# Performance work log

Measured on AMD Instinct MI355X. Metric: run time of the kernel, lower is better.

Reference implementation:

```python
import jax, jax.numpy as jnp
import numpy as np

N_NODE = 100000
HIDDEN = 128
BATCH = 4096
SESS_LEN = 50


def setup_inputs() -> dict:
    key = jax.random.key(0)
    k1, k2, k3, k4, k5 = jax.random.split(key, 5)
    return {
        "item_embedding": jax.random.normal(k1, (N_NODE, HIDDEN), dtype=jnp.float32),
        "items": jax.random.randint(k2, (BATCH, SESS_LEN), 0, N_NODE, dtype=jnp.int64),
        "A": jax.random.uniform(k3, (BATCH, BATCH), dtype=jnp.float32),
        "D": jax.random.uniform(k4, (BATCH, BATCH), dtype=jnp.float32),
        "target_embedding": jax.random.normal(k5, (BATCH, 1, 2 * HIDDEN), dtype=jnp.float32),
    }


def reference(item_embedding, items, A, D, target_embedding):
    # Gather per-session item embeddings: (batch, sess_len, hidden)
    seq_h = item_embedding[items]
    # Sum over session positions -> (batch, hidden)
    relation_emb = jnp.sum(seq_h, axis=1)
    # DA = D @ A, then propagate: (batch, batch) @ (batch, hidden)
    DA = jnp.matmul(D, A)
    relation_emb = jnp.matmul(DA, relation_emb)
    # Row-wise L2 normalization (torch.norm(dim=-1))
    norm = jnp.linalg.norm(relation_emb, axis=-1, keepdims=True)
    return relation_emb / norm
```

## Files before the change

kernel.cpp:

```cpp
#include <hip/hip_runtime.h>
#include <hip/hip_bf16.h>

#define BATCH   4096
#define HIDDEN  128
#define SESS    50
#define KTOT    4096
#define NB      ((size_t)BATCH * HIDDEN)

typedef __bf16 bf16x8 __attribute__((ext_vector_type(8)));
typedef float  f32x4  __attribute__((ext_vector_type(4)));
typedef unsigned char uchar;

__device__ __forceinline__ f32x4 mfma_bf16(bf16x8 a, bf16x8 b, f32x4 c) {
    return __builtin_amdgcn_mfma_f32_16x16x32_bf16(a, b, c, 0, 0, 0);
}

__device__ __forceinline__ long packBH(int k, int h) {
    return ((long)(k >> 3) << 10) + ((h >> 4) << 7) + ((h & 15) << 3) + (k & 7);
}

__global__ __launch_bounds__(64)
void probe_kernel(int* __restrict__ flag, uchar* __restrict__ rtab,
                  uchar* __restrict__ ctab) {
    __shared__ float As[16][32];
    __shared__ float Bs[32][16];
    __shared__ int cnt[256];
    const int lane = threadIdx.x;
    for (int idx = lane; idx < 512; idx += 64) {
        const int m = idx >> 5, k = idx & 31;
        As[m][k] = (float)(((m * 5 + k * 3) % 17) - 8);
        const int kb = idx >> 4, n = idx & 15;
        Bs[kb][n] = (float)(((kb * 7 + n * 11) % 17) - 8);
    }
    for (int i = lane; i < 256; i += 64) cnt[i] = 0;
    __syncthreads();

    const int lo = lane & 15, quad = lane >> 4;
    bf16x8 a, b, a1, b1, a2, b2;
#pragma unroll
    for (int j = 0; j < 8; ++j) {
        a[j]  = (__bf16)As[lo][quad * 8 + j];
        b[j]  = (__bf16)Bs[quad * 8 + j][lo];
        a1[j] = (__bf16)0.f; b1[j] = (__bf16)0.f;
        a2[j] = (__bf16)0.f; b2[j] = (__bf16)0.f;
    }
    if (quad == 0) {
        a1[0] = (__bf16)(float)lo;  b1[0] = (__bf16)1.f;
        a2[0] = (__bf16)1.f;        b2[0] = (__bf16)(float)lo;
    }
    const f32x4 z = {0.f, 0.f, 0.f, 0.f};
    f32x4 d  = mfma_bf16(a,  b,  z);
    f32x4 d1 = mfma_bf16(a1, b1, z);
    f32x4 d2 = mfma_bf16(a2, b2, z);

    bool ok = true;
    int ms[4], ns[4];
#pragma unroll
    for (int r = 0; r < 4; ++r) {
        const int m = (int)d1[r], n = (int)d2[r];
        ok = ok && ((float)m == d1[r]) && ((float)n == d2[r]) &&
             (m >= 0) && (m < 16) && (n >= 0) && (n < 16);
        ms[r] = m & 15; ns[r] = n & 15;
        float ref = 0.f;
        for (int k = 0; k < 32; ++k) ref += As[ms[r]][k] * Bs[k][ns[r]];
        ok = ok && (d[r] == ref);
        atomicAdd(&cnt[ms[r] * 16 + ns[r]], 1);
    }
    __syncthreads();
    bool comp = true;
    for (int i = lane; i < 256; i += 64) comp = comp && (cnt[i] == 1);

    const unsigned long long b_ok   = __ballot(ok);
    const unsigned long long b_comp = __ballot(comp);
#pragma unroll
    for (int r = 0; r < 4; ++r) {
        rtab[lane * 4 + r] = (uchar)ms[r];
        ctab[lane * 4 + r] = (uchar)ns[r];
    }
    if (lane == 0)
        *flag = (b_ok == ~0ULL && b_comp == ~0ULL) ? 1 : 0;
}

__global__ __launch_bounds__(256)
void gather_sum_kernel(const float* __restrict__ emb,
                       const int* __restrict__ items32,
                       float* __restrict__ Ef,
                       __bf16* __restrict__ ETp) {
    __shared__ int sidx[2][SESS];
    __shared__ f32x4 red[2][4][32];
    const int t  = threadIdx.x;
    const int b0 = blockIdx.x * 2;
    const bool is64 = (items32[1] | items32[3] | items32[5] | items32[7] |
                       items32[9] | items32[11] | items32[13] | items32[15]) == 0;
    if (t < 2 * SESS) {
        sidx[t / SESS][t % SESS] =
            is64 ? (int)((const long long*)items32)[(long)b0 * SESS + t]
                 : items32[b0 * SESS + t];
    }
    __syncthreads();
    const int r  = t >> 7;
    const int g  = (t >> 5) & 3;
    const int c4 = (t & 31) * 4;
    f32x4 acc = {0.f, 0.f, 0.f, 0.f};
#pragma unroll
    for (int s = g; s < SESS; s += 4) {
        acc += *(const f32x4*)(emb + (long)sidx[r][s] * HIDDEN + c4);
    }
    red[r][g][t & 31] = acc;
    __syncthreads();
    if (g == 0) {
        const int b = b0 + r;
        const f32x4 v = red[r][0][t & 31] + red[r][1][t & 31] +
                        red[r][2][t & 31] + red[r][3][t & 31];
        *(f32x4*)(Ef + (long)b * HIDDEN + c4) = v;
        const long pb = ((long)(b >> 3) << 10) + (b & 7) + ((c4 >> 4) << 7);
#pragma unroll
        for (int j = 0; j < 4; ++j)
            ETp[pb + ((c4 & 15) + j) * 8] = (__bf16)v[j];
    }
}

template <int PHASE>
__global__ __launch_bounds__(256, 4)
void gemm_mfma_kernel(const float* __restrict__ X,
                      const __bf16* __restrict__ BTp,
                      const int* __restrict__ flag,
                      const uchar* __restrict__ rtab,
                      const uchar* __restrict__ ctab,
                      float* __restrict__ Tp,
                      float* __restrict__ RpX) {
    if (*flag != 1) return;
    __shared__ float red[4][16][128];

    const int tid  = threadIdx.x;
    const int wave = tid >> 6;
    const int lane = tid & 63;
    const int lo   = lane & 15;
    const int quad = lane >> 4;
    const int rowBase = blockIdx.x * 16;
    const int sy      = blockIdx.y;
    const int kBase   = sy * 1024 + wave * 256;

    const unsigned rt4 = ((const unsigned*)rtab)[lane];
    const unsigned ct4 = ((const unsigned*)ctab)[lane];

    f32x4 acc[8];
#pragma unroll
    for (int i = 0; i < 8; ++i) acc[i] = (f32x4){0.f, 0.f, 0.f, 0.f};

    const float*  ap = X + (long)(rowBase + lo) * KTOT + kBase + quad * 8;
    const __bf16* bp = BTp + (((long)(kBase >> 3) + quad) << 10) + lo * 8;

    f32x4 x0 = *(const f32x4*)(ap);
    f32x4 x1 = *(const f32x4*)(ap + 4);
    bf16x8 bb[8];
#pragma unroll
    for (int nt = 0; nt < 8; ++nt)
        bb[nt] = *(const bf16x8*)(bp + nt * 128);

#pragma unroll
    for (int it = 0; it < 7; ++it) {
        const float*  ap2 = ap + (it + 1) * 32;
        const __bf16* bp2 = bp + (long)(it + 1) * 4096;
        const f32x4 nx0 = *(const f32x4*)(ap2);
        const f32x4 nx1 = *(const f32x4*)(ap2 + 4);
        bf16x8 nb[8];
#pragma unroll
        for (int nt = 0; nt < 8; ++nt)
            nb[nt] = *(const bf16x8*)(bp2 + nt * 128);
        bf16x8 a;
        a[0] = (__bf16)x0[0]; a[1] = (__bf16)x0[1];
        a[2] = (__bf16)x0[2]; a[3] = (__bf16)x0[3];
        a[4] = (__bf16)x1[0]; a[5] = (__bf16)x1[1];
        a[6] = (__bf16)x1[2]; a[7] = (__bf16)x1[3];
#pragma unroll
        for (int nt = 0; nt < 8; ++nt)
            acc[nt] = mfma_bf16(a, bb[nt], acc[nt]);
        x0 = nx0; x1 = nx1;
#pragma unroll
        for (int nt = 0; nt < 8; ++nt) bb[nt] = nb[nt];
    }
    {
        bf16x8 a;
        a[0] = (__bf16)x0[0]; a[1] = (__bf16)x0[1];
        a[2] = (__bf16)x0[2]; a[3] = (__bf16)x0[3];
        a[4] = (__bf16)x1[0]; a[5] = (__bf16)x1[1];
        a[6] = (__bf16)x1[2]; a[7] = (__bf16)x1[3];
#pragma unroll
        for (int nt = 0; nt < 8; ++nt)
            acc[nt] = mfma_bf16(a, bb[nt], acc[nt]);
    }

#pragma unroll
    for (int r = 0; r < 4; ++r) {
        const int dr = (rt4 >> (8 * r)) & 255;
        const int dc = (ct4 >> (8 * r)) & 255;
#pragma unroll
        for (int nt = 0; nt < 8; ++nt)
            red[wave][dr][nt * 16 + dc] = acc[nt][r];
    }
    __syncthreads();

    float* outp = (PHASE == 1) ? (Tp + (size_t)sy * NB)
                               : (sy < 3 ? Tp + (size_t)(sy + 1) * NB : RpX);
    const int row = tid >> 4;
    const int cb  = (tid & 15) * 8;
    f32x4 v0, v1;
#pragma unroll
    for (int j = 0; j < 4; ++j) {
        v0[j] = red[0][row][cb + j] + red[1][row][cb + j] +
                red[2][row][cb + j] + red[3][row][cb + j];
        v1[j] = red[0][row][cb + 4 + j] + red[1][row][cb + 4 + j] +
                red[2][row][cb + 4 + j] + red[3][row][cb + 4 + j];
    }
    *(f32x4*)(outp + (long)(rowBase + row) * HIDDEN + cb)     = v0;
    *(f32x4*)(outp + (long)(rowBase + row) * HIDDEN + cb + 4) = v1;
}

template <int PHASE>
__global__ __launch_bounds__(256)
void gemm_fp32_kernel(const float* __restrict__ X,
                      const float* __restrict__ B,
                      const int* __restrict__ flag,
                      float* __restrict__ Tp,
                      float* __restrict__ RpX) {
    if (*flag == 1) return;
    const int tid = threadIdx.x;
    const int cg4 = (tid & 31) * 4;
    const int rg  = tid >> 5;
    const int r0  = blockIdx.x * 32 + rg * 4;
    const int sy  = blockIdx.y;
    const int ks  = sy * 1024;
    float* outp = (PHASE == 1) ? (Tp + (size_t)sy * NB)
                               : (sy < 3 ? Tp + (size_t)(sy + 1) * NB : RpX);

    f32x4 acc[4];
#pragma unroll
    for (int j = 0; j < 4; ++j) acc[j] = (f32x4){0.f, 0.f, 0.f, 0.f};

    const float* Bp = B + (long)ks * HIDDEN + cg4;
    const float* Xp = X + (long)r0 * KTOT + ks;

    for (int k = 0; k < 1024; k += 4) {
        const f32x4 b0 = *(const f32x4*)(Bp + (long)(k + 0) * HIDDEN);
        const f32x4 b1 = *(const f32x4*)(Bp + (long)(k + 1) * HIDDEN);
        const f32x4 b2 = *(const f32x4*)(Bp + (long)(k + 2) * HIDDEN);
        const f32x4 b3 = *(const f32x4*)(Bp + (long)(k + 3) * HIDDEN);
#pragma unroll
        for (int j = 0; j < 4; ++j) {
            const f32x4 x = *(const f32x4*)(Xp + (long)j * KTOT + k);
            acc[j] += x[0] * b0;
            acc[j] += x[1] * b1;
            acc[j] += x[2] * b2;
            acc[j] += x[3] * b3;
        }
    }
#pragma unroll
    for (int j = 0; j < 4; ++j)
        *(f32x4*)(outp + (long)(r0 + j) * HIDDEN + cg4) = acc[j];
}

__global__ __launch_bounds__(256)
void reduce4_kernel(float* __restrict__ Tp, __bf16* __restrict__ TTp) {
    const size_t i = ((size_t)blockIdx.x * 256 + threadIdx.x) * 4;
    f32x4 a = *(const f32x4*)(Tp + i);
    a += *(const f32x4*)(Tp + NB + i);
    a += *(const f32x4*)(Tp + 2 * NB + i);
    a += *(const f32x4*)(Tp + 3 * NB + i);
    *(f32x4*)(Tp + i) = a;
    const int b  = (int)(i >> 7);
    const int h0 = (int)(i & 127);
    const long pb = ((long)(b >> 3) << 10) + (b & 7) + ((h0 >> 4) << 7);
#pragma unroll
    for (int j = 0; j < 4; ++j)
        TTp[pb + ((h0 & 15) + j) * 8] = (__bf16)a[j];
}

__global__ __launch_bounds__(128)
void reduce_norm_kernel(const float* __restrict__ Tp,
                        const float* __restrict__ RpX,
                        float* __restrict__ out) {
    __shared__ float s[128];
    const int row = blockIdx.x;
    const int h   = threadIdx.x;
    const size_t i = (size_t)row * HIDDEN + h;
    const float v = Tp[NB + i] + Tp[2 * NB + i] + Tp[3 * NB + i] + RpX[i];
    s[h] = v * v;
    __syncthreads();
#pragma unroll
    for (int o = 64; o > 0; o >>= 1) {
        if (h < o) s[h] += s[h + o];
        __syncthreads();
    }
    out[i] = v * rsqrtf(s[0]);
}

extern "C" void kernel_launch(void* const* d_in, const int* in_sizes, int n_in,
                              void* d_out, int out_size, void* d_ws, size_t ws_size,
                              hipStream_t stream) {
    const float* emb   = (const float*)d_in[0];
    const int*   items = (const int*)d_in[1];
    const float* A     = (const float*)d_in[2];
    const float* D     = (const float*)d_in[3];
    float* out = (float*)d_out;

    uchar* base = (uchar*)d_ws;
    int*   flag = (int*)base;
    uchar* rtab = base + 64;
    uchar* ctab = base + 320;
    float*  Ef  = (float*)(base + 1024);
    __bf16* ETp = (__bf16*)(Ef + NB);
    __bf16* TTp = ETp + NB;
    float*  Tp  = (float*)(TTp + NB);
    float*  RpX = Tp + 4 * NB;

    probe_kernel<<<1, 64, 0, stream>>>(flag, rtab, ctab);
    gather_sum_kernel<<<BATCH / 2, 256, 0, stream>>>(emb, items, Ef, ETp);

    gemm_mfma_kernel<1><<<dim3(BATCH / 16, 4), 256, 0, stream>>>(A, ETp, flag, rtab, ctab, Tp, RpX);
    gemm_fp32_kernel<1><<<dim3(BATCH / 32, 4), 256, 0, stream>>>(A, Ef, flag, Tp, RpX);
    reduce4_kernel<<<512, 256, 0, stream>>>(Tp, TTp);

    gemm_mfma_kernel<2><<<dim3(BATCH / 16, 4), 256, 0, stream>>>(D, TTp, flag, rtab, ctab, Tp, RpX);
    gemm_fp32_kernel<2><<<dim3(BATCH / 32, 4), 256, 0, stream>>>(D, Tp, flag, Tp, RpX);
    reduce_norm_kernel<<<BATCH, 128, 0, stream>>>(Tp, RpX, out);
}
```

Baseline: 238.4 us.

## Drop MFMA probe and fp32 fallback, stage B via global_load_lds double buffering

Removes the runtime MFMA layout probe kernel and its flag-gated fp32 fallback GEMMs, hardcoding the 16x16x32 bf16 output layout. The GEMM now streams the packed bf16 B operand into LDS with async global_load_lds in a two-stage double buffer, using explicit waitcnt control to overlap loads with MFMAs. Gather-sum, reduce4 and the final norm kernel are also reworked to use wave shuffles instead of LDS reductions, and redundant fp32 outputs are no longer written. The cost is 64KB of LDS per block, with occupancy lowered to 2, and the loss of the fallback path if the assumed MFMA layout is wrong.

```diff
diff --git a/kernel.cpp b/kernel.cpp
--- a/kernel.cpp
+++ b/kernel.cpp
@@ -9,129 +9,61 @@
 
 typedef __bf16 bf16x8 __attribute__((ext_vector_type(8)));
 typedef float  f32x4  __attribute__((ext_vector_type(4)));
-typedef unsigned char uchar;
+typedef float  f32x2  __attribute__((ext_vector_type(2)));
 
 __device__ __forceinline__ f32x4 mfma_bf16(bf16x8 a, bf16x8 b, f32x4 c) {
     return __builtin_amdgcn_mfma_f32_16x16x32_bf16(a, b, c, 0, 0, 0);
 }
 
-__device__ __forceinline__ long packBH(int k, int h) {
-    return ((long)(k >> 3) << 10) + ((h >> 4) << 7) + ((h & 15) << 3) + (k & 7);
-}
-
-__global__ __launch_bounds__(64)
-void probe_kernel(int* __restrict__ flag, uchar* __restrict__ rtab,
-                  uchar* __restrict__ ctab) {
-    __shared__ float As[16][32];
-    __shared__ float Bs[32][16];
-    __shared__ int cnt[256];
-    const int lane = threadIdx.x;
-    for (int idx = lane; idx < 512; idx += 64) {
-        const int m = idx >> 5, k = idx & 31;
-        As[m][k] = (float)(((m * 5 + k * 3) % 17) - 8);
-        const int kb = idx >> 4, n = idx & 15;
-        Bs[kb][n] = (float)(((kb * 7 + n * 11) % 17) - 8);
-    }
-    for (int i = lane; i < 256; i += 64) cnt[i] = 0;
-    __syncthreads();
-
-    const int lo = lane & 15, quad = lane >> 4;
-    bf16x8 a, b, a1, b1, a2, b2;
-#pragma unroll
-    for (int j = 0; j < 8; ++j) {
-        a[j]  = (__bf16)As[lo][quad * 8 + j];
-        b[j]  = (__bf16)Bs[quad * 8 + j][lo];
-        a1[j] = (__bf16)0.f; b1[j] = (__bf16)0.f;
-        a2[j] = (__bf16)0.f; b2[j] = (__bf16)0.f;
-    }
-    if (quad == 0) {
-        a1[0] = (__bf16)(float)lo;  b1[0] = (__bf16)1.f;
-        a2[0] = (__bf16)1.f;        b2[0] = (__bf16)(float)lo;
-    }
-    const f32x4 z = {0.f, 0.f, 0.f, 0.f};
-    f32x4 d  = mfma_bf16(a,  b,  z);
-    f32x4 d1 = mfma_bf16(a1, b1, z);
-    f32x4 d2 = mfma_bf16(a2, b2, z);
-
-    bool ok = true;
-    int ms[4], ns[4];
-#pragma unroll
-    for (int r = 0; r < 4; ++r) {
-        const int m = (int)d1[r], n = (int)d2[r];
-        ok = ok && ((float)m == d1[r]) && ((float)n == d2[r]) &&
-             (m >= 0) && (m < 16) && (n >= 0) && (n < 16);
-        ms[r] = m & 15; ns[r] = n & 15;
-        float ref = 0.f;
-        for (int k = 0; k < 32; ++k) ref += As[ms[r]][k] * Bs[k][ns[r]];
-        ok = ok && (d[r] == ref);
-        atomicAdd(&cnt[ms[r] * 16 + ns[r]], 1);
-    }
-    __syncthreads();
-    bool comp = true;
-    for (int i = lane; i < 256; i += 64) comp = comp && (cnt[i] == 1);
-
-    const unsigned long long b_ok   = __ballot(ok);
-    const unsigned long long b_comp = __ballot(comp);
-#pragma unroll
-    for (int r = 0; r < 4; ++r) {
-        rtab[lane * 4 + r] = (uchar)ms[r];
-        ctab[lane * 4 + r] = (uchar)ns[r];
-    }
-    if (lane == 0)
-        *flag = (b_ok == ~0ULL && b_comp == ~0ULL) ? 1 : 0;
-}
+__device__ __forceinline__ void gload16(const void* g, void* l) {
+    __builtin_amdgcn_global_load_lds(
+        (const __attribute__((address_space(1))) void*)g,
+        (__attribute__((address_space(3))) void*)l, 16, 0, 0);
+}
+
 
 __global__ __launch_bounds__(256)
 void gather_sum_kernel(const float* __restrict__ emb,
                        const int* __restrict__ items32,
-                       float* __restrict__ Ef,
                        __bf16* __restrict__ ETp) {
-    __shared__ int sidx[2][SESS];
-    __shared__ f32x4 red[2][4][32];
+    __shared__ int sidx[4][SESS];
     const int t  = threadIdx.x;
-    const int b0 = blockIdx.x * 2;
+    const int b0 = blockIdx.x * 4;
     const bool is64 = (items32[1] | items32[3] | items32[5] | items32[7] |
                        items32[9] | items32[11] | items32[13] | items32[15]) == 0;
-    if (t < 2 * SESS) {
-        sidx[t / SESS][t % SESS] =
-            is64 ? (int)((const long long*)items32)[(long)b0 * SESS + t]
-                 : items32[b0 * SESS + t];
+    if (t < 4 * SESS) {
+        const int w_ = t / SESS, s_ = t % SESS;
+        sidx[w_][s_] = is64
+            ? (int)((const long long*)items32)[(long)(b0 + w_) * SESS + s_]
+            : items32[(b0 + w_) * SESS + s_];
     }
     __syncthreads();
-    const int r  = t >> 7;
-    const int g  = (t >> 5) & 3;
-    const int c4 = (t & 31) * 4;
+    const int w    = t >> 6;
+    const int lane = t & 63;
+    const int c    = lane & 31;
+    const int h    = lane >> 5;
     f32x4 acc = {0.f, 0.f, 0.f, 0.f};
 #pragma unroll
-    for (int s = g; s < SESS; s += 4) {
-        acc += *(const f32x4*)(emb + (long)sidx[r][s] * HIDDEN + c4);
-    }
-    red[r][g][t & 31] = acc;
-    __syncthreads();
-    if (g == 0) {
-        const int b = b0 + r;
-        const f32x4 v = red[r][0][t & 31] + red[r][1][t & 31] +
-                        red[r][2][t & 31] + red[r][3][t & 31];
-        *(f32x4*)(Ef + (long)b * HIDDEN + c4) = v;
-        const long pb = ((long)(b >> 3) << 10) + (b & 7) + ((c4 >> 4) << 7);
+    for (int i = 0; i < 25; ++i) {
+        acc += *(const f32x4*)(emb + (long)sidx[w][h + 2 * i] * HIDDEN + c * 4);
+    }
+#pragma unroll
+    for (int j = 0; j < 4; ++j) acc[j] += __shfl_xor(acc[j], 32, 64);
+    if (h == 0) {
+        const int b  = b0 + w;
+        const int h0 = c * 4;
+        const long pb = ((long)(b >> 3) << 10) + (b & 7) + ((h0 >> 4) << 7);
 #pragma unroll
         for (int j = 0; j < 4; ++j)
-            ETp[pb + ((c4 & 15) + j) * 8] = (__bf16)v[j];
-    }
-}
-
-template <int PHASE>
-__global__ __launch_bounds__(256, 4)
+            ETp[pb + ((h0 & 15) + j) * 8] = (__bf16)acc[j];
+    }
+}
+
+__global__ __launch_bounds__(256, 2)
 void gemm_mfma_kernel(const float* __restrict__ X,
-                      const __bf16* __restrict__ BTp,
-                      const int* __restrict__ flag,
-                      const uchar* __restrict__ rtab,
-                      const uchar* __restrict__ ctab,
-                      float* __restrict__ Tp,
-                      float* __restrict__ RpX) {
-    if (*flag != 1) return;
-    __shared__ float red[4][16][128];
-
+                      const __bf16* __restrict__ Bpk,
+                      float* __restrict__ Tp) {
+    __shared__ __align__(16) float raw[16384];
     const int tid  = threadIdx.x;
     const int wave = tid >> 6;
     const int lane = tid & 63;
@@ -141,133 +73,97 @@
     const int sy      = blockIdx.y;
     const int kBase   = sy * 1024 + wave * 256;
 
-    const unsigned rt4 = ((const unsigned*)rtab)[lane];
-    const unsigned ct4 = ((const unsigned*)ctab)[lane];
+    const float* apt   = X + (long)(rowBase + lo) * KTOT + kBase + quad * 8;
+    const char*  bsrc  = (const char*)Bpk + ((long)(kBase >> 3) << 11);
+    char*        sbase = (char*)raw + wave * 16384;
 
     f32x4 acc[8];
 #pragma unroll
     for (int i = 0; i < 8; ++i) acc[i] = (f32x4){0.f, 0.f, 0.f, 0.f};
 
-    const float*  ap = X + (long)(rowBase + lo) * KTOT + kBase + quad * 8;
-    const __bf16* bp = BTp + (((long)(kBase >> 3) + quad) << 10) + lo * 8;
-
-    f32x4 x0 = *(const f32x4*)(ap);
-    f32x4 x1 = *(const f32x4*)(ap + 4);
-    bf16x8 bb[8];
-#pragma unroll
-    for (int nt = 0; nt < 8; ++nt)
-        bb[nt] = *(const bf16x8*)(bp + nt * 128);
-
-#pragma unroll
-    for (int it = 0; it < 7; ++it) {
-        const float*  ap2 = ap + (it + 1) * 32;
-        const __bf16* bp2 = bp + (long)(it + 1) * 4096;
-        const f32x4 nx0 = *(const f32x4*)(ap2);
-        const f32x4 nx1 = *(const f32x4*)(ap2 + 4);
-        bf16x8 nb[8];
+    f32x4 xa0[2], xa1[2];
+
+#define STAGE(ks_, cur_) do {                                                \
+    const char* g_ = bsrc + (ks_) * 8192 + lane * 16;                        \
+    char* l_ = sbase + (cur_) * 8192;                                        \
+    _Pragma("unroll")                                                        \
+    for (int i_ = 0; i_ < 8; ++i_)                                           \
+        gload16(g_ + i_ * 1024, l_ + i_ * 1024);                             \
+} while (0)
+
+    xa0[0] = *(const f32x4*)(apt);
+    xa1[0] = *(const f32x4*)(apt + 4);
+    STAGE(0, 0);
+    xa0[1] = *(const f32x4*)(apt + 32);
+    xa1[1] = *(const f32x4*)(apt + 36);
+    STAGE(1, 1);
+
+#define GITER(ks_, cur_, WAIT_, PRE_) do {                                   \
+    asm volatile(WAIT_ ::: "memory");                                        \
+    bf16x8 bb[8];                                                            \
+    _Pragma("unroll")                                                        \
+    for (int nt_ = 0; nt_ < 8; ++nt_)                                        \
+        bb[nt_] = *(const bf16x8*)(sbase + (cur_) * 8192 + quad * 2048 +     \
+                                   nt_ * 256 + lo * 16);                     \
+    bf16x8 a;                                                                \
+    a[0] = (__bf16)xa0[cur_][0]; a[1] = (__bf16)xa0[cur_][1];                \
+    a[2] = (__bf16)xa0[cur_][2]; a[3] = (__bf16)xa0[cur_][3];                \
+    a[4] = (__bf16)xa1[cur_][0]; a[5] = (__bf16)xa1[cur_][1];                \
+    a[6] = (__bf16)xa1[cur_][2]; a[7] = (__bf16)xa1[cur_][3];                \
+    asm volatile("s_waitcnt lgkmcnt(0)" ::: "memory");                       \
+    __builtin_amdgcn_sched_barrier(0);                                       \
+    if (PRE_) {                                                              \
+        xa0[cur_] = *(const f32x4*)(apt + ((ks_) + 2) * 32);                 \
+        xa1[cur_] = *(const f32x4*)(apt + ((ks_) + 2) * 32 + 4);             \
+        STAGE((ks_) + 2, cur_);                                              \
+    }                                                                        \
+    _Pragma("unroll")                                                        \
+    for (int nt_ = 0; nt_ < 8; ++nt_)                                        \
+        acc[nt_] = mfma_bf16(a, bb[nt_], acc[nt_]);                          \
+} while (0)
+
+    GITER(0, 0, "s_waitcnt vmcnt(10)", 1);
+    GITER(1, 1, "s_waitcnt vmcnt(10)", 1);
+    GITER(2, 0, "s_waitcnt vmcnt(10)", 1);
+    GITER(3, 1, "s_waitcnt vmcnt(10)", 1);
+    GITER(4, 0, "s_waitcnt vmcnt(10)", 1);
+    GITER(5, 1, "s_waitcnt vmcnt(10)", 1);
+    GITER(6, 0, "s_waitcnt vmcnt(10)", 0);
+    GITER(7, 1, "s_waitcnt vmcnt(0)",  0);
+
+#undef GITER
+#undef STAGE
+
+    __syncthreads();
+    float (*red)[16][132] = (float (*)[16][132])raw;
+#pragma unroll
+    for (int r = 0; r < 4; ++r) {
+        const int dr = quad * 4 + r;
 #pragma unroll
         for (int nt = 0; nt < 8; ++nt)
-            nb[nt] = *(const bf16x8*)(bp2 + nt * 128);
-        bf16x8 a;
-        a[0] = (__bf16)x0[0]; a[1] = (__bf16)x0[1];
-        a[2] = (__bf16)x0[2]; a[3] = (__bf16)x0[3];
-        a[4] = (__bf16)x1[0]; a[5] = (__bf16)x1[1];
-        a[6] = (__bf16)x1[2]; a[7] = (__bf16)x1[3];
-#pragma unroll
-        for (int nt = 0; nt < 8; ++nt)
-            acc[nt] = mfma_bf16(a, bb[nt], acc[nt]);
-        x0 = nx0; x1 = nx1;
-#pragma unroll
-        for (int nt = 0; nt < 8; ++nt) bb[nt] = nb[nt];
-    }
-    {
-        bf16x8 a;
-        a[0] = (__bf16)x0[0]; a[1] = (__bf16)x0[1];
-        a[2] = (__bf16)x0[2]; a[3] = (__bf16)x0[3];
-        a[4] = (__bf16)x1[0]; a[5] = (__bf16)x1[1];
-        a[6] = (__bf16)x1[2]; a[7] = (__bf16)x1[3];
-#pragma unroll
-        for (int nt = 0; nt < 8; ++nt)
-            acc[nt] = mfma_bf16(a, bb[nt], acc[nt]);
-    }
-
-#pragma unroll
-    for (int r = 0; r < 4; ++r) {
-        const int dr = (rt4 >> (8 * r)) & 255;
-        const int dc = (ct4 >> (8 * r)) & 255;
-#pragma unroll
-        for (int nt = 0; nt < 8; ++nt)
-            red[wave][dr][nt * 16 + dc] = acc[nt][r];
+            red[wave][dr][nt * 16 + lo] = acc[nt][r];
     }
     __syncthreads();
-
-    float* outp = (PHASE == 1) ? (Tp + (size_t)sy * NB)
-                               : (sy < 3 ? Tp + (size_t)(sy + 1) * NB : RpX);
     const int row = tid >> 4;
     const int cb  = (tid & 15) * 8;
-    f32x4 v0, v1;
-#pragma unroll
-    for (int j = 0; j < 4; ++j) {
-        v0[j] = red[0][row][cb + j] + red[1][row][cb + j] +
-                red[2][row][cb + j] + red[3][row][cb + j];
-        v1[j] = red[0][row][cb + 4 + j] + red[1][row][cb + 4 + j] +
-                red[2][row][cb + 4 + j] + red[3][row][cb + 4 + j];
-    }
-    *(f32x4*)(outp + (long)(rowBase + row) * HIDDEN + cb)     = v0;
-    *(f32x4*)(outp + (long)(rowBase + row) * HIDDEN + cb + 4) = v1;
-}
-
-template <int PHASE>
+    f32x4 v0 = {0.f, 0.f, 0.f, 0.f}, v1 = {0.f, 0.f, 0.f, 0.f};
+#pragma unroll
+    for (int w = 0; w < 4; ++w) {
+        v0 += *(const f32x4*)&red[w][row][cb];
+        v1 += *(const f32x4*)&red[w][row][cb + 4];
+    }
+    float* outp = Tp + (size_t)sy * NB + (long)(rowBase + row) * HIDDEN + cb;
+    *(f32x4*)(outp)     = v0;
+    *(f32x4*)(outp + 4) = v1;
+}
+
 __global__ __launch_bounds__(256)
-void gemm_fp32_kernel(const float* __restrict__ X,
-                      const float* __restrict__ B,
-                      const int* __restrict__ flag,
-                      float* __restrict__ Tp,
-                      float* __restrict__ RpX) {
-    if (*flag == 1) return;
-    const int tid = threadIdx.x;
-    const int cg4 = (tid & 31) * 4;
-    const int rg  = tid >> 5;
-    const int r0  = blockIdx.x * 32 + rg * 4;
-    const int sy  = blockIdx.y;
-    const int ks  = sy * 1024;
-    float* outp = (PHASE == 1) ? (Tp + (size_t)sy * NB)
-                               : (sy < 3 ? Tp + (size_t)(sy + 1) * NB : RpX);
-
-    f32x4 acc[4];
-#pragma unroll
-    for (int j = 0; j < 4; ++j) acc[j] = (f32x4){0.f, 0.f, 0.f, 0.f};
-
-    const float* Bp = B + (long)ks * HIDDEN + cg4;
-    const float* Xp = X + (long)r0 * KTOT + ks;
-
-    for (int k = 0; k < 1024; k += 4) {
-        const f32x4 b0 = *(const f32x4*)(Bp + (long)(k + 0) * HIDDEN);
-        const f32x4 b1 = *(const f32x4*)(Bp + (long)(k + 1) * HIDDEN);
-        const f32x4 b2 = *(const f32x4*)(Bp + (long)(k + 2) * HIDDEN);
-        const f32x4 b3 = *(const f32x4*)(Bp + (long)(k + 3) * HIDDEN);
-#pragma unroll
-        for (int j = 0; j < 4; ++j) {
-            const f32x4 x = *(const f32x4*)(Xp + (long)j * KTOT + k);
-            acc[j] += x[0] * b0;
-            acc[j] += x[1] * b1;
-            acc[j] += x[2] * b2;
-            acc[j] += x[3] * b3;
-        }
-    }
-#pragma unroll
-    for (int j = 0; j < 4; ++j)
-        *(f32x4*)(outp + (long)(r0 + j) * HIDDEN + cg4) = acc[j];
-}
-
-__global__ __launch_bounds__(256)
-void reduce4_kernel(float* __restrict__ Tp, __bf16* __restrict__ TTp) {
+void reduce4_kernel(const float* __restrict__ Tp, __bf16* __restrict__ TTp) {
     const size_t i = ((size_t)blockIdx.x * 256 + threadIdx.x) * 4;
     f32x4 a = *(const f32x4*)(Tp + i);
     a += *(const f32x4*)(Tp + NB + i);
     a += *(const f32x4*)(Tp + 2 * NB + i);
     a += *(const f32x4*)(Tp + 3 * NB + i);
-    *(f32x4*)(Tp + i) = a;
     const int b  = (int)(i >> 7);
     const int h0 = (int)(i & 127);
     const long pb = ((long)(b >> 3) << 10) + (b & 7) + ((h0 >> 4) << 7);
@@ -276,23 +172,23 @@
         TTp[pb + ((h0 & 15) + j) * 8] = (__bf16)a[j];
 }
 
-__global__ __launch_bounds__(128)
-void reduce_norm_kernel(const float* __restrict__ Tp,
-                        const float* __restrict__ RpX,
-                        float* __restrict__ out) {
-    __shared__ float s[128];
-    const int row = blockIdx.x;
-    const int h   = threadIdx.x;
-    const size_t i = (size_t)row * HIDDEN + h;
-    const float v = Tp[NB + i] + Tp[2 * NB + i] + Tp[3 * NB + i] + RpX[i];
-    s[h] = v * v;
-    __syncthreads();
-#pragma unroll
-    for (int o = 64; o > 0; o >>= 1) {
-        if (h < o) s[h] += s[h + o];
-        __syncthreads();
-    }
-    out[i] = v * rsqrtf(s[0]);
+__global__ __launch_bounds__(256)
+void reduce_norm_kernel(const float* __restrict__ Tp, float* __restrict__ out) {
+    const int t    = threadIdx.x;
+    const int w    = t >> 6;
+    const int lane = t & 63;
+    const int row  = blockIdx.x * 4 + w;
+    const size_t base = (size_t)row * HIDDEN + lane * 2;
+    f32x2 v = *(const f32x2*)(Tp + base);
+    v += *(const f32x2*)(Tp + NB + base);
+    v += *(const f32x2*)(Tp + 2 * NB + base);
+    v += *(const f32x2*)(Tp + 3 * NB + base);
+    float sq = v[0] * v[0] + v[1] * v[1];
+#pragma unroll
+    for (int m = 1; m < 64; m <<= 1) sq += __shfl_xor(sq, m, 64);
+    const float s = rsqrtf(sq);
+    f32x2 o = {v[0] * s, v[1] * s};
+    *(f32x2*)(out + base) = o;
 }
 
 extern "C" void kernel_launch(void* const* d_in, const int* in_sizes, int n_in,
@@ -304,24 +200,15 @@
     const float* D     = (const float*)d_in[3];
     float* out = (float*)d_out;
 
-    uchar* base = (uchar*)d_ws;
-    int*   flag = (int*)base;
-    uchar* rtab = base + 64;
-    uchar* ctab = base + 320;
-    float*  Ef  = (float*)(base + 1024);
-    __bf16* ETp = (__bf16*)(Ef + NB);
+    __bf16* ETp = (__bf16*)d_ws;
     __bf16* TTp = ETp + NB;
     float*  Tp  = (float*)(TTp + NB);
-    float*  RpX = Tp + 4 * NB;
-
-    probe_kernel<<<1, 64, 0, stream>>>(flag, rtab, ctab);
-    gather_sum_kernel<<<BATCH / 2, 256, 0, stream>>>(emb, items, Ef, ETp);
-
-    gemm_mfma_kernel<1><<<dim3(BATCH / 16, 4), 256, 0, stream>>>(A, ETp, flag, rtab, ctab, Tp, RpX);
-    gemm_fp32_kernel<1><<<dim3(BATCH / 32, 4), 256, 0, stream>>>(A, Ef, flag, Tp, RpX);
+
+    gather_sum_kernel<<<BATCH / 4, 256, 0, stream>>>(emb, items, ETp);
+
+    gemm_mfma_kernel<<<dim3(BATCH / 16, 4), 256, 0, stream>>>(A, ETp, Tp);
     reduce4_kernel<<<512, 256, 0, stream>>>(Tp, TTp);
 
-    gemm_mfma_kernel<2><<<dim3(BATCH / 16, 4), 256, 0, stream>>>(D, TTp, flag, rtab, ctab, Tp, RpX);
-    gemm_fp32_kernel<2><<<dim3(BATCH / 32, 4), 256, 0, stream>>>(D, Tp, flag, Tp, RpX);
-    reduce_norm_kernel<<<BATCH, 128, 0, stream>>>(Tp, RpX, out);
-}
+    gemm_mfma_kernel<<<dim3(BATCH / 16, 4), 256, 0, stream>>>(D, TTp, Tp);
+    reduce_norm_kernel<<<BATCH / 4, 256, 0, stream>>>(Tp, out);
+}
```

Result: faster. 229.4 us (-3.7%).
